# Performance work log

Measured on AMD Instinct MI355X. Metric: run time of the kernel, lower is better.

Reference implementation:

```python
import jax, jax.numpy as jnp
import numpy as np

NA = 100000  # number of a-type nodes (rows of adj)
NB = 100000  # number of b-type nodes (cols of adj)
NE = 1600000 # number of edges (nnz of adj)
BF = 128     # b_features
AF = 128     # a_features


def setup_inputs() -> dict:
    key = jax.random.key(0)
    k1, k2, k3, k4, k5, k6 = jax.random.split(key, 6)
    stdv = 1.0 / np.sqrt(BF)
    return {
        "b_input": jax.random.normal(k1, (NB, BF), dtype=jnp.float32),
        "edge_rows": jax.random.randint(k2, (NE,), 0, NA, dtype=jnp.int32),
        "edge_cols": jax.random.randint(k3, (NE,), 0, NB, dtype=jnp.int32),
        "edge_vals": jax.random.uniform(k4, (NE,), dtype=jnp.float32),
        "a_weight": jax.random.uniform(k5, (BF, AF), minval=-stdv, maxval=stdv, dtype=jnp.float32),
        "a_bias": jax.random.uniform(k6, (AF,), minval=-stdv, maxval=stdv, dtype=jnp.float32),
    }


def reference(b_input, edge_rows, edge_cols, edge_vals, a_weight, a_bias):
    # a_support = b_input @ a_weight            : [NB, AF]
    a_support = jnp.matmul(b_input, a_weight)
    # a_output = spmm(adj, a_support)           : [NA, AF]
    # adj[r, c] = edge_vals at (edge_rows, edge_cols)
    gathered = a_support[edge_cols] * edge_vals[:, None]   # [NE, AF]
    a_output = jax.ops.segment_sum(gathered, edge_rows, num_segments=NA)
    # bias=True -> early return of a-side output
    return a_output + a_bias
```

## Files before the change

### kernel.cpp

```cpp
#include <hip/hip_runtime.h>
#include <hip/hip_bf16.h>

#define AF 128
#define BF 128
#define BROWS 64
#define CAP_F 1600
#define CROWS 1024
#define CAP_C 18432
#define CHUNK1 2048
#define NCOARSE_MAX 128

typedef __attribute__((ext_vector_type(8))) short bf16x8;
typedef __attribute__((ext_vector_type(4))) float f32x4;

__device__ inline unsigned short f2bf(float f) {
    unsigned int u = __float_as_uint(f);
    u += 0x7FFF + ((u >> 16) & 1);
    return (unsigned short)(u >> 16);
}
__device__ inline unsigned int pk2bf(float x, float y) {
    __hip_bfloat162 h = __float22bfloat162_rn(make_float2(x, y));
    return *(unsigned int*)&h;
}
__device__ inline float bflo(unsigned int u) { return __uint_as_float(u << 16); }
__device__ inline float bfhi(unsigned int u) { return __uint_as_float(u & 0xFFFF0000u); }

__global__ void wtrans_kernel(const float* __restrict__ W, unsigned short* __restrict__ Wt) {
    int idx = blockIdx.x * 256 + threadIdx.x;
    int n = idx & 127, k = idx >> 7;
    Wt[n * 128 + k] = f2bf(W[(size_t)k * 128 + n]);
}

__global__ __launch_bounds__(256) void gemm_mfma_kernel(const float* __restrict__ Bin,
                                                        const unsigned short* __restrict__ Wt,
                                                        unsigned int* __restrict__ Sup, int NB) {
    __shared__ unsigned short Ws[128][136];
    const int tid = threadIdx.x;
    const int lane = tid & 63;
    const int wave = tid >> 6;
    const int row0 = blockIdx.x * 64;
    const int m = lane & 15;
    const int quad = lane >> 4;

    {
        int r = tid >> 1;
        int c = (tid & 1) * 64;
        const uint4* src = (const uint4*)(Wt + r * 128 + c);
        uint4* dst = (uint4*)(&Ws[r][c]);
        #pragma unroll
        for (int i = 0; i < 8; i++) dst[i] = src[i];
    }

    int arow = row0 + wave * 16 + m;
    int arow_c = (arow < NB) ? arow : (NB - 1);
    const float* ap = Bin + (size_t)arow_c * BF + quad * 8;
    bf16x8 af[4];
    #pragma unroll
    for (int ks = 0; ks < 4; ks++) {
        float4 lo = *(const float4*)(ap + ks * 32);
        float4 hi = *(const float4*)(ap + ks * 32 + 4);
        union { unsigned int u[4]; bf16x8 v; } cv;
        cv.u[0] = pk2bf(lo.x, lo.y); cv.u[1] = pk2bf(lo.z, lo.w);
        cv.u[2] = pk2bf(hi.x, hi.y); cv.u[3] = pk2bf(hi.z, hi.w);
        af[ks] = cv.v;
    }
    __syncthreads();

    f32x4 acc[8];
    #pragma unroll
    for (int nt = 0; nt < 8; nt++) {
        f32x4 a = {0.f, 0.f, 0.f, 0.f};
        #pragma unroll
        for (int ks = 0; ks < 4; ks++) {
            bf16x8 bf = *(const bf16x8*)(&Ws[nt * 16 + m][ks * 32 + quad * 8]);
            a = __builtin_amdgcn_mfma_f32_16x16x32_bf16(af[ks], bf, a, 0, 0, 0);
        }
        acc[nt] = a;
    }
    #pragma unroll
    for (int nt = 0; nt < 4; nt++) {
        #pragma unroll
        for (int r = 0; r < 4; r++) {
            int row = row0 + wave * 16 + quad * 4 + r;
            if (row < NB)
                Sup[(size_t)row * 64 + nt * 16 + m] = pk2bf(acc[nt][r], acc[nt + 4][r]);
        }
    }
}

__global__ __launch_bounds__(256) void passA1_kernel(const int* __restrict__ rows,
                                                     const int* __restrict__ cols,
                                                     const float* __restrict__ vals,
                                                     int* __restrict__ grelC,
                                                     int2* __restrict__ binnedC, int NE, int NCOARSE) {
    __shared__ int h[NCOARSE_MAX];
    __shared__ int rbase[NCOARSE_MAX];
    int tid = threadIdx.x;
    if (tid < NCOARSE) h[tid] = 0;
    __syncthreads();
    int base = blockIdx.x * CHUNK1;
    #pragma unroll
    for (int i = 0; i < CHUNK1 / 256; i++) {
        int e = base + tid + i * 256;
        if (e < NE) atomicAdd(&h[rows[e] >> 10], 1);
    }
    __syncthreads();
    if (tid < NCOARSE) {
        int c = h[tid];
        rbase[tid] = tid * CAP_C + (c ? atomicAdd(&grelC[tid], c) : 0);
        h[tid] = 0;
    }
    __syncthreads();
    #pragma unroll
    for (int i = 0; i < CHUNK1 / 256; i++) {
        int e = base + tid + i * 256;
        if (e < NE) {
            int r = rows[e];
            int k = r >> 10;
            int lp = atomicAdd(&h[k], 1);
            int2 p;
            p.x = cols[e] | ((r & 1023) << 17);
            p.y = __float_as_int(vals[e]);
            binnedC[rbase[k] + lp] = p;
        }
    }
}

__global__ __launch_bounds__(256) void passA2_kernel(const int2* __restrict__ binnedC,
                                                     const int* __restrict__ grelC,
                                                     int* __restrict__ grelF,
                                                     int2* __restrict__ binnedF, int NBUCK) {
    __shared__ int h[16];
    __shared__ int rb[16];
    const int tid = threadIdx.x;
    const int j = blockIdx.x >> 3;
    const int s = blockIdx.x & 7;
    int n = grelC[j]; if (n > CAP_C) n = CAP_C;
    const int st = (n * s) >> 3;
    const int en = (n * (s + 1)) >> 3;
    const int2* src = binnedC + (size_t)j * CAP_C;
    if (tid < 16) h[tid] = 0;
    __syncthreads();
    for (int i = st + tid; i < en; i += 256)
        atomicAdd(&h[src[i].x >> 23], 1);
    __syncthreads();
    if (tid < 16) {
        int c = h[tid];
        int fine = j * 16 + tid;
        rb[tid] = (fine < NBUCK) ? (fine * CAP_F + (c ? atomicAdd(&grelF[fine], c) : 0)) : 0;
        h[tid] = 0;
    }
    __syncthreads();
    for (int i = st + tid; i < en; i += 256) {
        int2 p = src[i];
        int sub = p.x >> 23;
        int lp = atomicAdd(&h[sub], 1);
        int2 q;
        q.x = p.x & 0x7FFFFF;
        q.y = p.y;
        binnedF[(size_t)rb[sub] + lp] = q;
    }
}

__global__ __launch_bounds__(256) void spmm_sorted_kernel(const unsigned short* __restrict__ Sup,
                                                          const int2* __restrict__ binned,
                                                          const int* __restrict__ grel,
                                                          const float* __restrict__ bias,
                                                          float* __restrict__ out, int NA) {
    __shared__ int   spx[CAP_F];
    __shared__ float spy[CAP_F];
    __shared__ int cnt[BROWS];
    __shared__ int sc[BROWS];
    __shared__ int rs[BROWS + 1];
    __shared__ int cur[BROWS];
    const int tid = threadIdx.x;
    const int b = blockIdx.x;
    int n = grel[b]; if (n > CAP_F) n = CAP_F;
    const int2* src = binned + (size_t)b * CAP_F;

    int2 pr[7];
    #pragma unroll
    for (int j = 0; j < 7; j++) {
        int i = tid + j * 256;
        pr[j] = (i < n) ? src[i] : make_int2(-1, 0);
    }
    if (tid < BROWS) cnt[tid] = 0;
    __syncthreads();
    #pragma unroll
    for (int j = 0; j < 7; j++)
        if (pr[j].x >= 0) atomicAdd(&cnt[(pr[j].x >> 17) & 63], 1);
    __syncthreads();
    int v = (tid < BROWS) ? cnt[tid] : 0;
    int x = v;
    if (tid < BROWS) sc[tid] = x;
    __syncthreads();
    #pragma unroll
    for (int off = 1; off < BROWS; off <<= 1) {
        int t = (tid < BROWS && tid >= off) ? sc[tid - off] : 0;
        __syncthreads();
        if (tid < BROWS) { x += t; sc[tid] = x; }
        __syncthreads();
    }
    if (tid < BROWS) { rs[tid] = x - v; cur[tid] = x - v; }
    if (tid == BROWS - 1) rs[BROWS] = x;
    __syncthreads();
    #pragma unroll
    for (int j = 0; j < 7; j++) {
        if (pr[j].x >= 0) {
            int lr = (pr[j].x >> 17) & 63;
            int pos = atomicAdd(&cur[lr], 1);
            spx[pos] = pr[j].x & 0x1FFFF;
            spy[pos] = __int_as_float(pr[j].y);
        }
    }
    __syncthreads();

    const int lane = tid & 63;
    const int wv = tid >> 6;
    const float b0 = bias[lane];
    const float b1 = bias[64 + lane];
    for (int lr = wv; lr < BROWS; lr += 4) {
        int row = b * BROWS + lr;
        if (row >= NA) break;
        int e = rs[lr], end = rs[lr + 1];
        float ax = 0.f, ay = 0.f;
        for (; e + 8 <= end; e += 8) {
            int c0 = spx[e],     c1 = spx[e + 1], c2 = spx[e + 2], c3 = spx[e + 3];
            int c4 = spx[e + 4], c5 = spx[e + 5], c6 = spx[e + 6], c7 = spx[e + 7];
            float v0 = spy[e],     v1 = spy[e + 1], v2 = spy[e + 2], v3 = spy[e + 3];
            float v4 = spy[e + 4], v5 = spy[e + 5], v6 = spy[e + 6], v7 = spy[e + 7];
            unsigned int s0 = *(const unsigned int*)(Sup + (size_t)c0 * AF + lane * 2);
            unsigned int s1 = *(const unsigned int*)(Sup + (size_t)c1 * AF + lane * 2);
            unsigned int s2 = *(const unsigned int*)(Sup + (size_t)c2 * AF + lane * 2);
            unsigned int s3 = *(const unsigned int*)(Sup + (size_t)c3 * AF + lane * 2);
            unsigned int s4 = *(const unsigned int*)(Sup + (size_t)c4 * AF + lane * 2);
            unsigned int s5 = *(const unsigned int*)(Sup + (size_t)c5 * AF + lane * 2);
            unsigned int s6 = *(const unsigned int*)(Sup + (size_t)c6 * AF + lane * 2);
            unsigned int s7 = *(const unsigned int*)(Sup + (size_t)c7 * AF + lane * 2);
            ax += v0 * bflo(s0) + v1 * bflo(s1) + v2 * bflo(s2) + v3 * bflo(s3)
                + v4 * bflo(s4) + v5 * bflo(s5) + v6 * bflo(s6) + v7 * bflo(s7);
            ay += v0 * bfhi(s0) + v1 * bfhi(s1) + v2 * bfhi(s2) + v3 * bfhi(s3)
                + v4 * bfhi(s4) + v5 * bfhi(s5) + v6 * bfhi(s6) + v7 * bfhi(s7);
        }
        for (; e < end; e++) {
            int c = spx[e];
            float vv = spy[e];
            unsigned int s = *(const unsigned int*)(Sup + (size_t)c * AF + lane * 2);
            ax += vv * bflo(s);
            ay += vv * bfhi(s);
        }
        out[(size_t)row * AF + lane]      = ax + b0;
        out[(size_t)row * AF + 64 + lane] = ay + b1;
    }
}

extern "C" void kernel_launch(void* const* d_in, const int* in_sizes, int n_in,
                              void* d_out, int out_size, void* d_ws, size_t ws_size,
                              hipStream_t stream) {
    const float* b_input   = (const float*)d_in[0];
    const int*   edge_rows = (const int*)d_in[1];
    const int*   edge_cols = (const int*)d_in[2];
    const float* edge_vals = (const float*)d_in[3];
    const float* a_weight  = (const float*)d_in[4];
    const float* a_bias    = (const float*)d_in[5];
    const int NB = in_sizes[0] / BF;
    const int NE = in_sizes[1];
    const int NA = out_size / AF;
    const int NBUCK = (NA + BROWS - 1) / BROWS;
    const int NCOARSE = (NA + CROWS - 1) / CROWS;
    float* out = (float*)d_out;

    char* ws = (char*)d_ws;
    size_t off = 0;
    unsigned short* Sup = (unsigned short*)(ws + off); off += (size_t)NB * AF * sizeof(unsigned short);
    unsigned short* Wt  = (unsigned short*)(ws + off); off += (size_t)BF * AF * sizeof(unsigned short);
    int* grelC = (int*)(ws + off); off += 1024 * sizeof(int);
    int* grelF = (int*)(ws + off); off += 2048 * sizeof(int);
    int2* binnedC = (int2*)(ws + off); off += (size_t)NCOARSE * CAP_C * sizeof(int2);
    int2* binnedF = (int2*)(ws + off); off += (size_t)NBUCK * CAP_F * sizeof(int2);
    (void)ws_size; (void)n_in;

    hipMemsetAsync(grelC, 0, 3072 * sizeof(int), stream);

    wtrans_kernel<<<64, 256, 0, stream>>>(a_weight, Wt);
    gemm_mfma_kernel<<<(NB + 63) / 64, 256, 0, stream>>>(b_input, Wt, (unsigned int*)Sup, NB);
    passA1_kernel<<<(NE + CHUNK1 - 1) / CHUNK1, 256, 0, stream>>>(
        edge_rows, edge_cols, edge_vals, grelC, binnedC, NE, NCOARSE);
    passA2_kernel<<<NCOARSE * 8, 256, 0, stream>>>(binnedC, grelC, grelF, binnedF, NBUCK);
    spmm_sorted_kernel<<<NBUCK, 256, 0, stream>>>(Sup, binnedF, grelF, a_bias, out, NA);
}
```

Before: 235.5 us.

## Fuse GEMM and coarse binning into one launch; pad row segments to eight

Merges the weight transpose, the MFMA GEMM and the first binning pass into a single kernel whose blocks split by index into GEMM work or edge binning. This removes two launches and lets the two independent phases run concurrently on the GPU. Each GEMM block now converts and transposes the fp32 weight into LDS itself, which repeats that work in every block. In the SpMM kernel, column and value are packed into one int2 LDS array, and each row's segment is padded to a multiple of eight with zero entries so the scalar tail loop disappears, at the cost of extra zero-weight gathers.

New measurement: 233.0 us. No clear change (-1.0%).

```diff
diff --git a/kernel.cpp b/kernel.cpp
--- a/kernel.cpp
+++ b/kernel.cpp
@@ -5,6 +5,7 @@
 #define BF 128
 #define BROWS 64
 #define CAP_F 1600
+#define SORT_CAP 1664
 #define CROWS 1024
 #define CAP_C 18432
 #define CHUNK1 2048
@@ -25,103 +26,105 @@
 __device__ inline float bflo(unsigned int u) { return __uint_as_float(u << 16); }
 __device__ inline float bfhi(unsigned int u) { return __uint_as_float(u & 0xFFFF0000u); }
 
-__global__ void wtrans_kernel(const float* __restrict__ W, unsigned short* __restrict__ Wt) {
-    int idx = blockIdx.x * 256 + threadIdx.x;
-    int n = idx & 127, k = idx >> 7;
-    Wt[n * 128 + k] = f2bf(W[(size_t)k * 128 + n]);
-}
-
-__global__ __launch_bounds__(256) void gemm_mfma_kernel(const float* __restrict__ Bin,
-                                                        const unsigned short* __restrict__ Wt,
-                                                        unsigned int* __restrict__ Sup, int NB) {
-    __shared__ unsigned short Ws[128][136];
-    const int tid = threadIdx.x;
-    const int lane = tid & 63;
-    const int wave = tid >> 6;
-    const int row0 = blockIdx.x * 64;
-    const int m = lane & 15;
-    const int quad = lane >> 4;
-
-    {
-        int r = tid >> 1;
-        int c = (tid & 1) * 64;
-        const uint4* src = (const uint4*)(Wt + r * 128 + c);
-        uint4* dst = (uint4*)(&Ws[r][c]);
-        #pragma unroll
-        for (int i = 0; i < 8; i++) dst[i] = src[i];
-    }
-
-    int arow = row0 + wave * 16 + m;
-    int arow_c = (arow < NB) ? arow : (NB - 1);
-    const float* ap = Bin + (size_t)arow_c * BF + quad * 8;
-    bf16x8 af[4];
-    #pragma unroll
-    for (int ks = 0; ks < 4; ks++) {
-        float4 lo = *(const float4*)(ap + ks * 32);
-        float4 hi = *(const float4*)(ap + ks * 32 + 4);
-        union { unsigned int u[4]; bf16x8 v; } cv;
-        cv.u[0] = pk2bf(lo.x, lo.y); cv.u[1] = pk2bf(lo.z, lo.w);
-        cv.u[2] = pk2bf(hi.x, hi.y); cv.u[3] = pk2bf(hi.z, hi.w);
-        af[ks] = cv.v;
-    }
-    __syncthreads();
-
-    f32x4 acc[8];
-    #pragma unroll
-    for (int nt = 0; nt < 8; nt++) {
-        f32x4 a = {0.f, 0.f, 0.f, 0.f};
-        #pragma unroll
-        for (int ks = 0; ks < 4; ks++) {
-            bf16x8 bf = *(const bf16x8*)(&Ws[nt * 16 + m][ks * 32 + quad * 8]);
-            a = __builtin_amdgcn_mfma_f32_16x16x32_bf16(af[ks], bf, a, 0, 0, 0);
-        }
-        acc[nt] = a;
-    }
-    #pragma unroll
-    for (int nt = 0; nt < 4; nt++) {
-        #pragma unroll
-        for (int r = 0; r < 4; r++) {
-            int row = row0 + wave * 16 + quad * 4 + r;
-            if (row < NB)
-                Sup[(size_t)row * 64 + nt * 16 + m] = pk2bf(acc[nt][r], acc[nt + 4][r]);
-        }
-    }
-}
-
-__global__ __launch_bounds__(256) void passA1_kernel(const int* __restrict__ rows,
+__global__ __launch_bounds__(256) void phase1_kernel(const float* __restrict__ Bin,
+                                                     const float* __restrict__ W,
+                                                     unsigned int* __restrict__ Sup, int NB,
+                                                     const int* __restrict__ rows,
                                                      const int* __restrict__ cols,
                                                      const float* __restrict__ vals,
                                                      int* __restrict__ grelC,
-                                                     int2* __restrict__ binnedC, int NE, int NCOARSE) {
+                                                     int2* __restrict__ binnedC,
+                                                     int NE, int NCOARSE, int ngemm) {
+    __shared__ unsigned short Ws[128][136];
     __shared__ int h[NCOARSE_MAX];
     __shared__ int rbase[NCOARSE_MAX];
-    int tid = threadIdx.x;
-    if (tid < NCOARSE) h[tid] = 0;
-    __syncthreads();
-    int base = blockIdx.x * CHUNK1;
-    #pragma unroll
-    for (int i = 0; i < CHUNK1 / 256; i++) {
-        int e = base + tid + i * 256;
-        if (e < NE) atomicAdd(&h[rows[e] >> 10], 1);
-    }
-    __syncthreads();
-    if (tid < NCOARSE) {
-        int c = h[tid];
-        rbase[tid] = tid * CAP_C + (c ? atomicAdd(&grelC[tid], c) : 0);
-        h[tid] = 0;
-    }
-    __syncthreads();
-    #pragma unroll
-    for (int i = 0; i < CHUNK1 / 256; i++) {
-        int e = base + tid + i * 256;
-        if (e < NE) {
-            int r = rows[e];
-            int k = r >> 10;
-            int lp = atomicAdd(&h[k], 1);
-            int2 p;
-            p.x = cols[e] | ((r & 1023) << 17);
-            p.y = __float_as_int(vals[e]);
-            binnedC[rbase[k] + lp] = p;
+    const int tid = threadIdx.x;
+
+    if ((int)blockIdx.x < ngemm) {
+        const int lane = tid & 63;
+        const int wave = tid >> 6;
+        const int row0 = blockIdx.x * 64;
+        const int m = lane & 15;
+        const int quad = lane >> 4;
+
+        {
+            int k = tid >> 1;
+            int n0 = (tid & 1) * 64;
+            const float4* src = (const float4*)(W + (size_t)k * AF + n0);
+            #pragma unroll
+            for (int i = 0; i < 16; i++) {
+                float4 v = src[i];
+                int n = n0 + i * 4;
+                Ws[n + 0][k] = f2bf(v.x);
+                Ws[n + 1][k] = f2bf(v.y);
+                Ws[n + 2][k] = f2bf(v.z);
+                Ws[n + 3][k] = f2bf(v.w);
+            }
+        }
+        int arow = row0 + wave * 16 + m;
+        int arow_c = (arow < NB) ? arow : (NB - 1);
+        const float* ap = Bin + (size_t)arow_c * BF + quad * 8;
+        bf16x8 af[4];
+        #pragma unroll
+        for (int ks = 0; ks < 4; ks++) {
+            float4 lo = *(const float4*)(ap + ks * 32);
+            float4 hi = *(const float4*)(ap + ks * 32 + 4);
+            union { unsigned int u[4]; bf16x8 v; } cv;
+            cv.u[0] = pk2bf(lo.x, lo.y); cv.u[1] = pk2bf(lo.z, lo.w);
+            cv.u[2] = pk2bf(hi.x, hi.y); cv.u[3] = pk2bf(hi.z, hi.w);
+            af[ks] = cv.v;
+        }
+        __syncthreads();
+
+        f32x4 acc[8];
+        #pragma unroll
+        for (int nt = 0; nt < 8; nt++) {
+            f32x4 a = {0.f, 0.f, 0.f, 0.f};
+            #pragma unroll
+            for (int ks = 0; ks < 4; ks++) {
+                bf16x8 bf = *(const bf16x8*)(&Ws[nt * 16 + m][ks * 32 + quad * 8]);
+                a = __builtin_amdgcn_mfma_f32_16x16x32_bf16(af[ks], bf, a, 0, 0, 0);
+            }
+            acc[nt] = a;
+        }
+        #pragma unroll
+        for (int nt = 0; nt < 4; nt++) {
+            #pragma unroll
+            for (int r = 0; r < 4; r++) {
+                int row = row0 + wave * 16 + quad * 4 + r;
+                if (row < NB)
+                    Sup[(size_t)row * 64 + nt * 16 + m] = pk2bf(acc[nt][r], acc[nt + 4][r]);
+            }
+        }
+    } else {
+        int bid = blockIdx.x - ngemm;
+        if (tid < NCOARSE) h[tid] = 0;
+        __syncthreads();
+        int base = bid * CHUNK1;
+        #pragma unroll
+        for (int i = 0; i < CHUNK1 / 256; i++) {
+            int e = base + tid + i * 256;
+            if (e < NE) atomicAdd(&h[rows[e] >> 10], 1);
+        }
+        __syncthreads();
+        if (tid < NCOARSE) {
+            int c = h[tid];
+            rbase[tid] = tid * CAP_C + (c ? atomicAdd(&grelC[tid], c) : 0);
+            h[tid] = 0;
+        }
+        __syncthreads();
+        #pragma unroll
+        for (int i = 0; i < CHUNK1 / 256; i++) {
+            int e = base + tid + i * 256;
+            if (e < NE) {
+                int r = rows[e];
+                int k = r >> 10;
+                int lp = atomicAdd(&h[k], 1);
+                int2 p;
+                p.x = cols[e] | ((r & 1023) << 17);
+                p.y = __float_as_int(vals[e]);
+                binnedC[rbase[k] + lp] = p;
+            }
         }
     }
 }
@@ -167,8 +170,7 @@
                                                           const int* __restrict__ grel,
                                                           const float* __restrict__ bias,
                                                           float* __restrict__ out, int NA) {
-    __shared__ int   spx[CAP_F];
-    __shared__ float spy[CAP_F];
+    __shared__ int2 spxy[SORT_CAP];
     __shared__ int cnt[BROWS];
     __shared__ int sc[BROWS];
     __shared__ int rs[BROWS + 1];
@@ -190,7 +192,7 @@
     for (int j = 0; j < 7; j++)
         if (pr[j].x >= 0) atomicAdd(&cnt[(pr[j].x >> 17) & 63], 1);
     __syncthreads();
-    int v = (tid < BROWS) ? cnt[tid] : 0;
+    int v = (tid < BROWS) ? ((cnt[tid] + 7) & ~7) : 0;
     int x = v;
     if (tid < BROWS) sc[tid] = x;
     __syncthreads();
@@ -209,9 +211,13 @@
         if (pr[j].x >= 0) {
             int lr = (pr[j].x >> 17) & 63;
             int pos = atomicAdd(&cur[lr], 1);
-            spx[pos] = pr[j].x & 0x1FFFF;
-            spy[pos] = __int_as_float(pr[j].y);
-        }
+            spxy[pos] = make_int2(pr[j].x & 0x1FFFF, pr[j].y);
+        }
+    }
+    __syncthreads();
+    if (tid < BROWS) {
+        int end = rs[tid + 1];
+        for (int p = cur[tid]; p < end; p++) spxy[p] = make_int2(0, 0);
     }
     __syncthreads();
 
@@ -224,30 +230,25 @@
         if (row >= NA) break;
         int e = rs[lr], end = rs[lr + 1];
         float ax = 0.f, ay = 0.f;
-        for (; e + 8 <= end; e += 8) {
-            int c0 = spx[e],     c1 = spx[e + 1], c2 = spx[e + 2], c3 = spx[e + 3];
-            int c4 = spx[e + 4], c5 = spx[e + 5], c6 = spx[e + 6], c7 = spx[e + 7];
-            float v0 = spy[e],     v1 = spy[e + 1], v2 = spy[e + 2], v3 = spy[e + 3];
-            float v4 = spy[e + 4], v5 = spy[e + 5], v6 = spy[e + 6], v7 = spy[e + 7];
-            unsigned int s0 = *(const unsigned int*)(Sup + (size_t)c0 * AF + lane * 2);
-            unsigned int s1 = *(const unsigned int*)(Sup + (size_t)c1 * AF + lane * 2);
-            unsigned int s2 = *(const unsigned int*)(Sup + (size_t)c2 * AF + lane * 2);
-            unsigned int s3 = *(const unsigned int*)(Sup + (size_t)c3 * AF + lane * 2);
-            unsigned int s4 = *(const unsigned int*)(Sup + (size_t)c4 * AF + lane * 2);
-            unsigned int s5 = *(const unsigned int*)(Sup + (size_t)c5 * AF + lane * 2);
-            unsigned int s6 = *(const unsigned int*)(Sup + (size_t)c6 * AF + lane * 2);
-            unsigned int s7 = *(const unsigned int*)(Sup + (size_t)c7 * AF + lane * 2);
+        for (; e < end; e += 8) {
+            int2 q0 = spxy[e],     q1 = spxy[e + 1], q2 = spxy[e + 2], q3 = spxy[e + 3];
+            int2 q4 = spxy[e + 4], q5 = spxy[e + 5], q6 = spxy[e + 6], q7 = spxy[e + 7];
+            unsigned int s0 = *(const unsigned int*)(Sup + (size_t)q0.x * AF + lane * 2);
+            unsigned int s1 = *(const unsigned int*)(Sup + (size_t)q1.x * AF + lane * 2);
+            unsigned int s2 = *(const unsigned int*)(Sup + (size_t)q2.x * AF + lane * 2);
+            unsigned int s3 = *(const unsigned int*)(Sup + (size_t)q3.x * AF + lane * 2);
+            unsigned int s4 = *(const unsigned int*)(Sup + (size_t)q4.x * AF + lane * 2);
+            unsigned int s5 = *(const unsigned int*)(Sup + (size_t)q5.x * AF + lane * 2);
+            unsigned int s6 = *(const unsigned int*)(Sup + (size_t)q6.x * AF + lane * 2);
+            unsigned int s7 = *(const unsigned int*)(Sup + (size_t)q7.x * AF + lane * 2);
+            float v0 = __int_as_float(q0.y), v1 = __int_as_float(q1.y);
+            float v2 = __int_as_float(q2.y), v3 = __int_as_float(q3.y);
+            float v4 = __int_as_float(q4.y), v5 = __int_as_float(q5.y);
+            float v6 = __int_as_float(q6.y), v7 = __int_as_float(q7.y);
             ax += v0 * bflo(s0) + v1 * bflo(s1) + v2 * bflo(s2) + v3 * bflo(s3)
                 + v4 * bflo(s4) + v5 * bflo(s5) + v6 * bflo(s6) + v7 * bflo(s7);
             ay += v0 * bfhi(s0) + v1 * bfhi(s1) + v2 * bfhi(s2) + v3 * bfhi(s3)
                 + v4 * bfhi(s4) + v5 * bfhi(s5) + v6 * bfhi(s6) + v7 * bfhi(s7);
-        }
-        for (; e < end; e++) {
-            int c = spx[e];
-            float vv = spy[e];
-            unsigned int s = *(const unsigned int*)(Sup + (size_t)c * AF + lane * 2);
-            ax += vv * bflo(s);
-            ay += vv * bfhi(s);
         }
         out[(size_t)row * AF + lane]      = ax + b0;
         out[(size_t)row * AF + 64 + lane] = ay + b1;
@@ -273,7 +274,6 @@
     char* ws = (char*)d_ws;
     size_t off = 0;
     unsigned short* Sup = (unsigned short*)(ws + off); off += (size_t)NB * AF * sizeof(unsigned short);
-    unsigned short* Wt  = (unsigned short*)(ws + off); off += (size_t)BF * AF * sizeof(unsigned short);
     int* grelC = (int*)(ws + off); off += 1024 * sizeof(int);
     int* grelF = (int*)(ws + off); off += 2048 * sizeof(int);
     int2* binnedC = (int2*)(ws + off); off += (size_t)NCOARSE * CAP_C * sizeof(int2);
@@ -282,10 +282,11 @@
 
     hipMemsetAsync(grelC, 0, 3072 * sizeof(int), stream);
 
-    wtrans_kernel<<<64, 256, 0, stream>>>(a_weight, Wt);
-    gemm_mfma_kernel<<<(NB + 63) / 64, 256, 0, stream>>>(b_input, Wt, (unsigned int*)Sup, NB);
-    passA1_kernel<<<(NE + CHUNK1 - 1) / CHUNK1, 256, 0, stream>>>(
-        edge_rows, edge_cols, edge_vals, grelC, binnedC, NE, NCOARSE);
+    const int ngemm = (NB + 63) / 64;
+    const int npass = (NE + CHUNK1 - 1) / CHUNK1;
+    phase1_kernel<<<ngemm + npass, 256, 0, stream>>>(
+        b_input, a_weight, (unsigned int*)Sup, NB,
+        edge_rows, edge_cols, edge_vals, grelC, binnedC, NE, NCOARSE, ngemm);
     passA2_kernel<<<NCOARSE * 8, 256, 0, stream>>>(binnedC, grelC, grelF, binnedF, NBUCK);
     spmm_sorted_kernel<<<NBUCK, 256, 0, stream>>>(Sup, binnedF, grelF, a_bias, out, NA);
 }
```
